# Optimization experiments

Measured on AMD Instinct MI355X. Metric: run time of the kernel, lower is better.

The kernel has to match this reference:

```python
import jax, jax.numpy as jnp
import numpy as np
import math
from jax import lax

D = 256      # d_model = out_channel
NH = 8       # n_heads
DEP = D // NH
DFF = 1024
B = 48       # conv batch == attended axis in this model
CIN = 32
HW = 32
S = 30 * 30  # (HW-2)**2 after 3x3 valid conv
OUT = 1
FMAX = float(np.finfo(np.float32).max)


def _p(k, shp, scale=0.02):
    return jax.random.normal(k, shp, jnp.float32) * scale


def setup_inputs():
    key = jax.random.key(0)
    ks = jax.random.split(key, 34)
    return {
        'X_en': jax.random.normal(ks[0], (B, CIN, HW, HW), jnp.float32),
        'X_de': jax.random.normal(ks[1], (B, CIN, HW, HW), jnp.float32),
        'conv1_w': _p(ks[2], (D, CIN, 3, 3)), 'conv1_b': _p(ks[3], (D,)),
        'conv2_w': _p(ks[4], (D, D, 3, 3)), 'conv2_b': _p(ks[5], (D,)),
        'enc_wq': _p(ks[6], (D, D)), 'enc_wk': _p(ks[7], (D, D)), 'enc_wv': _p(ks[8], (D, D)),
        'enc_rel_w': _p(ks[9], (S, NH, DEP, B)),
        'enc_ffn_w1': _p(ks[10], (DFF, D)), 'enc_ffn_b1': _p(ks[11], (DFF,)),
        'enc_ffn_w2': _p(ks[12], (D, DFF)), 'enc_ffn_b2': _p(ks[13], (D,)),
        'dec_m_wq': _p(ks[14], (D, D)), 'dec_m_wk': _p(ks[15], (D, D)), 'dec_m_wv': _p(ks[16], (D, D)),
        'dec_m_rel_w': _p(ks[17], (S, NH, DEP, B)),
        'dec_m_lin1_w': _p(ks[18], (B, B)), 'dec_m_lin1_b': _p(ks[19], (B,)),
        'dec_m_lin2_w': _p(ks[20], (B, B)), 'dec_m_lin2_b': _p(ks[21], (B,)),
        'dec_c_wq': _p(ks[22], (D, D)), 'dec_c_wk': _p(ks[23], (D, D)), 'dec_c_wv': _p(ks[24], (D, D)),
        'dec_c_rel_w': _p(ks[25], (S, NH, DEP, B)),
        'dec_ffn_w1': _p(ks[26], (DFF, D)), 'dec_ffn_b1': _p(ks[27], (DFF,)),
        'dec_ffn_w2': _p(ks[28], (D, DFF)), 'dec_ffn_b2': _p(ks[29], (D,)),
        'out_w': _p(ks[30], (OUT, D)), 'out_b': _p(ks[31], (OUT,)),
    }


def _ln(x, eps=1e-5):
    m = jnp.mean(x, -1, keepdims=True)
    v = jnp.mean((x - m) ** 2, -1, keepdims=True)
    return (x - m) / jnp.sqrt(v + eps)


def _skew(q, w):
    # Music-Transformer relative-position skew: matmul + pad + reshape + slice
    emd = jnp.einsum('shbd,shdj->shbj', q, w)  # (S,NH,b,b)
    s, h, i, j = emd.shape
    l = i + j - 1
    x = jnp.concatenate([emd, jnp.zeros_like(emd)], -1).reshape(s, h, -1)
    pad = (-x.shape[-1]) % l
    x = jnp.pad(x, ((0, 0), (0, 0), (0, pad)))
    return x.reshape(s, h, -1, l)[:, :, :i, i - 1:]


def _mha(xq, xk, xv, wq, wk, wv, rel_w, lins=None):
    b, sl, d = xq.shape
    # raw view (not transpose): (b,sl,d) -> (sl,b,NH,DEP), then swap to (sl,NH,b,DEP)
    q = (xq @ wq.T).reshape(sl, b, NH, DEP).swapaxes(1, 2)
    k = (xk @ wk.T).reshape(sl, b, NH, DEP).swapaxes(1, 2)
    v = (xv @ wv.T).reshape(sl, b, NH, DEP).swapaxes(1, 2)
    scores = jnp.einsum('shid,shjd->shij', q, k) / math.sqrt(DEP)  # (sl,NH,b,b)
    if lins is not None:  # masked path: per-call linears + causal mask
        l1w, l1b, l2w, l2b = lins
        qk = scores @ l1w.T + l1b
        qk = jnp.swapaxes(qk, 2, 3) @ l2w.T + l2b
        mask = jnp.triu(jnp.full((b, b), -FMAX, jnp.float32), 1)
        bmm = qk + mask
    else:
        bmm = scores  # linear1/linear2 outputs are discarded when mask=False
    attn = jax.nn.softmax(bmm + _skew(q, rel_w), axis=0)  # softmax over dim 0 (S)
    out = jnp.einsum('shij,shjd->shid', attn, v)  # (sl,NH,b,DEP)
    return out.reshape(b, sl, NH * DEP)  # view(a_s[2], a_s[0], -1)


def reference(X_en, X_de, conv1_w, conv1_b, conv2_w, conv2_b, enc_wq, enc_wk, enc_wv, enc_rel_w, enc_ffn_w1, enc_ffn_b1, enc_ffn_w2, enc_ffn_b2, dec_m_wq, dec_m_wk, dec_m_wv, dec_m_rel_w, dec_m_lin1_w, dec_m_lin1_b, dec_m_lin2_w, dec_m_lin2_b, dec_c_wq, dec_c_wk, dec_c_wv, dec_c_rel_w, dec_ffn_w1, dec_ffn_b1, dec_ffn_w2, dec_ffn_b2, out_w, out_b):
    def conv(x, w, b_, pad):
        y = lax.conv_general_dilated(x, w, (1, 1), [(pad, pad), (pad, pad)],
                                     dimension_numbers=('NCHW', 'OIHW', 'NCHW'))
        return y + b_[None, :, None, None]

    def convs(x):
        return conv(conv(x, conv1_w, conv1_b, 0), conv2_w, conv2_b, 1)

    xpe = convs(X_en)
    xpd = convs(X_de)
    b, d, h, w = xpe.shape
    x_en = xpe.reshape(b, h * w, d)  # raw reshape as in torch source
    x_de = xpd.reshape(b, h * w, d)
    # encoder layer
    a = _mha(x_en, x_en, x_en, enc_wq, enc_wk, enc_wv, enc_rel_w)
    o1 = _ln(x_en + a)
    f = jax.nn.relu(o1 @ enc_ffn_w1.T + enc_ffn_b1) @ enc_ffn_w2.T + enc_ffn_b2
    enc_out = _ln(o1 + f)
    # decoder layer
    m = _mha(x_de, x_de, x_de, dec_m_wq, dec_m_wk, dec_m_wv, dec_m_rel_w,
             (dec_m_lin1_w, dec_m_lin1_b, dec_m_lin2_w, dec_m_lin2_b))
    h1 = _ln(x_de + m)
    c = _mha(h1, enc_out, enc_out, dec_c_wq, dec_c_wk, dec_c_wv, dec_c_rel_w)
    h2 = _ln(c + h1)
    f2 = jax.nn.relu(h2 @ dec_ffn_w1.T + dec_ffn_b1) @ dec_ffn_w2.T + dec_ffn_b2
    h3 = _ln(h2 + f2)
    y = h3 @ out_w.T + out_b
    return jax.nn.softmax(y, axis=0)
```

## Files before the change

### kernel.cpp

```cpp
#include <hip/hip_runtime.h>
#include <float.h>

typedef __bf16 bf16;
typedef __attribute__((ext_vector_type(8))) __bf16 bf16x8;
typedef __attribute__((ext_vector_type(4))) __bf16 bf16x4;
typedef __attribute__((ext_vector_type(4))) float f32x4;

__device__ __forceinline__ int imin(int a, int b) { return a < b ? a : b; }

__device__ __forceinline__ void gl2lds(const bf16* g, bf16* l) {
  __builtin_amdgcn_global_load_lds(
      (const __attribute__((address_space(1))) void*)g,
      (__attribute__((address_space(3))) void*)l, 16, 0, 0);
}

__global__ void k_zero(bf16* zp) { zp[threadIdx.x] = (bf16)0.0f; }

struct CastSegs { const float* s[13]; bf16* d[13]; int n[13]; };
__global__ void k_cast_all(CastSegs sg, int total) {
  int i = blockIdx.x * 256 + threadIdx.x;
  if (i >= total) return;
  for (int k = 0; k < 13; ++k) {
    if (i < sg.n[k]) { sg.d[k][i] = (bf16)sg.s[k][i]; return; }
    i -= sg.n[k];
  }
}

__global__ void k_prep_x(const float* __restrict__ X, bf16* __restrict__ XR) {
  int idx = blockIdx.x * 256 + threadIdx.x;
  if (idx >= 48 * 1024 * 32) return;
  int b = idx >> 15, r = idx & 32767, pos = r >> 5, ic = r & 31;
  XR[idx] = (bf16)X[((size_t)(b * 32 + ic) << 10) + pos];
}

__global__ void k_pack_conv(const float* __restrict__ w, bf16* __restrict__ dst,
                            int OC, int IC, int total) {
  int idx = blockIdx.x * 256 + threadIdx.x;
  if (idx >= total) return;
  int t = idx / (OC * IC);
  int rem = idx - t * OC * IC;
  int oc = rem / IC, ic = rem - oc * IC;
  dst[idx] = (bf16)w[(size_t)(oc * IC + ic) * 9 + t];
}

__global__ __launch_bounds__(256, 2) void k_gemm128(
    const bf16* __restrict__ A, const bf16* __restrict__ B,
    const float* __restrict__ bias, bf16* __restrict__ C,
    int M, int N, int K, int relu, int ldc, int coff) {
  __shared__ alignas(16) bf16 SM[8192];
  bf16* As = SM;
  bf16* Bs = SM + 4096;
  const int t = threadIdx.x, wave = t >> 6;
  const int lane = t & 63, fr = lane & 15, kq = lane >> 4;
  const int wm = wave & 1, wn = wave >> 1;
  const int m0 = blockIdx.x * 128, n0 = blockIdx.y * 128;
  const int srow = t >> 2, kseg = (t & 3) * 8;
  f32x4 acc[4][4] = {};
  const bf16* gA0 = A + (size_t)imin(m0 + srow, M - 1) * K + kseg;
  const bf16* gA1 = A + (size_t)imin(m0 + 64 + srow, M - 1) * K + kseg;
  const bf16* gB0 = B + (size_t)(n0 + srow) * K + kseg;
  const bf16* gB1 = B + (size_t)(n0 + 64 + srow) * K + kseg;
  bf16* sA0 = As + wave * 512;
  bf16* sA1 = As + 2048 + wave * 512;
  bf16* sB0 = Bs + wave * 512;
  bf16* sB1 = Bs + 2048 + wave * 512;
  for (int k0 = 0; k0 < K; k0 += 32) {
    gl2lds(gA0 + k0, sA0);
    gl2lds(gA1 + k0, sA1);
    gl2lds(gB0 + k0, sB0);
    gl2lds(gB1 + k0, sB1);
    __syncthreads();
    bf16x8 af[4], bw[4];
    for (int mt = 0; mt < 4; ++mt)
      af[mt] = *(const bf16x8*)(As + (wm * 64 + mt * 16 + fr) * 32 + kq * 8);
    for (int nt = 0; nt < 4; ++nt)
      bw[nt] = *(const bf16x8*)(Bs + (wn * 64 + nt * 16 + fr) * 32 + kq * 8);
    for (int mt = 0; mt < 4; ++mt)
      for (int nt = 0; nt < 4; ++nt)
        acc[mt][nt] = __builtin_amdgcn_mfma_f32_16x16x32_bf16(af[mt], bw[nt], acc[mt][nt], 0, 0, 0);
    __syncthreads();
  }
  bf16* Cst = SM;
  for (int half = 0; half < 2; ++half) {
    if (wm == half) {
      for (int mt = 0; mt < 4; ++mt)
        for (int nt = 0; nt < 4; ++nt) {
          int n = n0 + wn * 64 + nt * 16 + fr;
          float bv = bias ? bias[n] : 0.0f;
          for (int r = 0; r < 4; ++r) {
            float v = acc[mt][nt][r] + bv;
            if (relu) v = fmaxf(v, 0.0f);
            Cst[(mt * 16 + kq * 4 + r) * 128 + wn * 64 + nt * 16 + fr] = (bf16)v;
          }
        }
    }
    __syncthreads();
    for (int i = t; i < 1024; i += 256) {
      int r = i >> 4, cs = i & 15;
      int gm = m0 + half * 64 + r;
      if (gm < M)
        *(bf16x8*)(C + (size_t)gm * ldc + coff + n0 + cs * 8) = *(const bf16x8*)(Cst + r * 128 + cs * 8);
    }
    __syncthreads();
  }
}

template <int CIN, int PAD, int SRCW, int SRCROWS, int CHECK, int TRANS>
__global__ __launch_bounds__(256, 2) void k_conv128(
    const bf16* __restrict__ A, const bf16* __restrict__ Bp,
    const float* __restrict__ bias, bf16* __restrict__ C,
    const bf16* __restrict__ zpage) {
  __shared__ alignas(16) bf16 SM[8192];
  bf16* As = SM;
  bf16* Bs = SM + 4096;
  const int t = threadIdx.x, wave = t >> 6;
  const int lane = t & 63, fr = lane & 15, kq = lane >> 4;
  const int wm = wave & 1, wn = wave >> 1;
  const int m0 = blockIdx.x * 128, n0 = blockIdx.y * 128;
  const int srow = t >> 2, kseg = (t & 3) * 8;
  f32x4 acc[4][4] = {};
  int bb[2], yy[2], xx[2];
  for (int hf = 0; hf < 2; ++hf) {
    int m = imin(m0 + hf * 64 + srow, 43199);
    int b = m / 900, p = m - b * 900;
    bb[hf] = b; yy[hf] = p / 30; xx[hf] = p - (p / 30) * 30;
  }
  bf16* sA0 = As + wave * 512;
  bf16* sA1 = As + 2048 + wave * 512;
  bf16* sB0 = Bs + wave * 512;
  bf16* sB1 = Bs + 2048 + wave * 512;
  for (int t9 = 0; t9 < 9; ++t9) {
    const int ky = t9 / 3, kx = t9 - ky * 3;
    const bf16* ga[2];
    for (int hf = 0; hf < 2; ++hf) {
      int sy = yy[hf] + ky - PAD, sx = xx[hf] + kx - PAD;
      bool valid = !CHECK || (sy >= 0 && sy < SRCW && sx >= 0 && sx < SRCW);
      ga[hf] = (valid ? A + (size_t)(bb[hf] * SRCROWS + sy * SRCW + sx) * CIN : zpage) + kseg;
    }
    const bf16* gb = Bp + (size_t)(t9 * 256 + n0 + srow) * CIN + kseg;
    for (int k0 = 0; k0 < CIN; k0 += 32) {
      gl2lds(ga[0] + k0, sA0);
      gl2lds(ga[1] + k0, sA1);
      gl2lds(gb + k0, sB0);
      gl2lds(gb + (size_t)64 * CIN + k0, sB1);
      __syncthreads();
      bf16x8 af[4], bw[4];
      for (int mt = 0; mt < 4; ++mt)
        af[mt] = *(const bf16x8*)(As + (wm * 64 + mt * 16 + fr) * 32 + kq * 8);
      for (int nt = 0; nt < 4; ++nt)
        bw[nt] = *(const bf16x8*)(Bs + (wn * 64 + nt * 16 + fr) * 32 + kq * 8);
      for (int mt = 0; mt < 4; ++mt)
        for (int nt = 0; nt < 4; ++nt)
          acc[mt][nt] = __builtin_amdgcn_mfma_f32_16x16x32_bf16(af[mt], bw[nt], acc[mt][nt], 0, 0, 0);
      __syncthreads();
    }
  }
  bf16* Cst = SM;
  for (int half = 0; half < 2; ++half) {
    if (wm == half) {
      for (int mt = 0; mt < 4; ++mt)
        for (int nt = 0; nt < 4; ++nt) {
          int n = n0 + wn * 64 + nt * 16 + fr;
          float bv = bias[n];
          for (int r = 0; r < 4; ++r) {
            float v = acc[mt][nt][r] + bv;
            if (TRANS)
              Cst[(wn * 64 + nt * 16 + fr) * 64 + mt * 16 + kq * 4 + r] = (bf16)v;
            else
              Cst[(mt * 16 + kq * 4 + r) * 128 + wn * 64 + nt * 16 + fr] = (bf16)v;
          }
        }
    }
    __syncthreads();
    if (TRANS) {
      for (int i = t; i < 2048; i += 256) {
        int oc = i >> 4, pc = i & 15;
        int gm = m0 + half * 64 + pc * 4;
        if (gm < 43200) {
          int b = gm / 900, p = gm - b * 900;
          *(bf16x4*)(C + (size_t)(b * 256 + n0 + oc) * 900 + p) = *(const bf16x4*)(Cst + oc * 64 + pc * 4);
        }
      }
    } else {
      for (int i = t; i < 1024; i += 256) {
        int r = i >> 4, cs = i & 15;
        int gm = m0 + half * 64 + r;
        if (gm < 43200)
          *(bf16x8*)(C + (size_t)gm * 256 + n0 + cs * 8) = *(const bf16x8*)(Cst + r * 128 + cs * 8);
      }
    }
    __syncthreads();
  }
}

template <int MASKED>
__global__ __launch_bounds__(256, MASKED ? 3 : 4) void k_attn_z(
    const bf16* __restrict__ QKV, const float* __restrict__ relw, bf16* __restrict__ Z,
    const float* __restrict__ l1w, const float* __restrict__ l1b,
    const float* __restrict__ l2w, const float* __restrict__ l2b) {
  __shared__ alignas(16) bf16 Rt[48 * 40];
  __shared__ float EMD[48 * 49];
  __shared__ alignas(16) bf16 zst[48 * 48];
  __shared__ alignas(16) bf16 Sc[MASKED ? 48 * 72 : 8];
  __shared__ alignas(16) bf16 L1b[MASKED ? 48 * 72 : 8];
  __shared__ alignas(16) bf16 L2b[MASKED ? 48 * 72 : 8];
  __shared__ alignas(16) bf16 T2b[MASKED ? 48 * 72 : 8];
  const int sh = blockIdx.x, s = sh >> 3, h = sh & 7;
  const int t = threadIdx.x, wave = t >> 6, lane = t & 63, fr = lane & 15, kq = lane >> 4;
  const float scale = 0.17677669529663687f;
  if constexpr (MASKED) {
    for (int i = t; i < 48 * 72; i += 256) {
      int r = i / 72, c = i - r * 72;
      bf16 z0 = (bf16)0.0f;
      L1b[i] = (c < 48) ? (bf16)l1w[r * 48 + c] : z0;
      L2b[i] = (c < 48) ? (bf16)l2w[r * 48 + c] : z0;
      Sc[i] = z0;
      T2b[i] = z0;
    }
  }
  {
    const float* rb = relw + (size_t)sh * 1536;
    for (int i = t; i < 1536; i += 256) {
      int k = i / 48, j = i - k * 48;
      Rt[j * 40 + k] = (bf16)rb[i];
    }
  }
  __syncthreads();
  f32x4 sreg[3];
  int u = 0;
  for (int t9 = wave; t9 < 9; t9 += 4, ++u) {
    int ti = t9 / 3, tj = t9 - ti * 3;
    bf16x8 af = *(const bf16x8*)(QKV + (size_t)(s * 48 + ti * 16 + fr) * 768 + h * 32 + kq * 8);
    bf16x8 bk = *(const bf16x8*)(QKV + (size_t)(s * 48 + tj * 16 + fr) * 768 + 256 + h * 32 + kq * 8);
    bf16x8 rf = *(const bf16x8*)(Rt + (tj * 16 + fr) * 40 + kq * 8);
    f32x4 sacc = {}, eacc = {};
    sacc = __builtin_amdgcn_mfma_f32_16x16x32_bf16(af, bk, sacc, 0, 0, 0);
    eacc = __builtin_amdgcn_mfma_f32_16x16x32_bf16(af, rf, eacc, 0, 0, 0);
    for (int r = 0; r < 4; ++r)
      EMD[(ti * 16 + kq * 4 + r) * 49 + tj * 16 + fr] = eacc[r];
    if constexpr (MASKED) {
      for (int r = 0; r < 4; ++r)
        Sc[(ti * 16 + kq * 4 + r) * 72 + tj * 16 + fr] = (bf16)(sacc[r] * scale);
    } else {
      for (int r = 0; r < 4; ++r) sreg[u][r] = sacc[r] * scale;
    }
  }
  __syncthreads();
  if constexpr (!MASKED) {
    u = 0;
    for (int t9 = wave; t9 < 9; t9 += 4, ++u) {
      int ti = t9 / 3, tj = t9 - ti * 3;
      for (int r = 0; r < 4; ++r) {
        int i = ti * 16 + kq * 4 + r, j = tj * 16 + fr;
        float v = sreg[u][r];
        if (j <= i) v += EMD[i * 49 + 47 + j - i];
        zst[i * 48 + j] = (bf16)v;
      }
    }
  } else {
    for (int t9 = wave; t9 < 9; t9 += 4) {
      int ti = t9 / 3, tj = t9 - ti * 3;
      f32x4 a2 = {};
      for (int k0 = 0; k0 < 64; k0 += 32) {
        bf16x8 af = *(const bf16x8*)(Sc + (ti * 16 + fr) * 72 + k0 + kq * 8);
        bf16x8 bw = *(const bf16x8*)(L1b + (tj * 16 + fr) * 72 + k0 + kq * 8);
        a2 = __builtin_amdgcn_mfma_f32_16x16x32_bf16(af, bw, a2, 0, 0, 0);
      }
      for (int r = 0; r < 4; ++r) {
        int i = ti * 16 + kq * 4 + r, a = tj * 16 + fr;
        T2b[a * 72 + i] = (bf16)(a2[r] + l1b[a]);
      }
    }
    __syncthreads();
    for (int t9 = wave; t9 < 9; t9 += 4) {
      int ti = t9 / 3, tj = t9 - ti * 3;
      f32x4 a2 = {};
      for (int k0 = 0; k0 < 64; k0 += 32) {
        bf16x8 af = *(const bf16x8*)(T2b + (ti * 16 + fr) * 72 + k0 + kq * 8);
        bf16x8 bw = *(const bf16x8*)(L2b + (tj * 16 + fr) * 72 + k0 + kq * 8);
        a2 = __builtin_amdgcn_mfma_f32_16x16x32_bf16(af, bw, a2, 0, 0, 0);
      }
      for (int r = 0; r < 4; ++r) {
        int aa = ti * 16 + kq * 4 + r, cc = tj * 16 + fr;
        float v;
        if (cc > aa) v = -10000.0f;
        else v = a2[r] + l2b[cc] + EMD[aa * 49 + 47 + cc - aa];
        zst[aa * 48 + cc] = (bf16)v;
      }
    }
  }
  __syncthreads();
  bf16* zb = Z + (size_t)sh * 2304;
  for (int c = t; c < 288; c += 256)
    *(bf16x8*)(zb + c * 8) = *(const bf16x8*)(zst + c * 8);
}

__global__ __launch_bounds__(256) void k_colstats(const bf16* __restrict__ Z,
                                                  float* __restrict__ Mc, float* __restrict__ Ic) {
  __shared__ float rm[4][64], rs[4][64];
  const int t = threadIdx.x, tc = t & 63, sg = t >> 6;
  const int col = blockIdx.x * 64 + tc;
  const bf16* p = Z + col;
  float m = -FLT_MAX, ssum = 0.0f;
  for (int s = sg * 225; s < sg * 225 + 225; ++s) {
    float v = (float)p[(size_t)s * 18432];
    if (v > m) { ssum *= __expf(m - v); m = v; }
    ssum += __expf(v - m);
  }
  rm[sg][tc] = m; rs[sg][tc] = ssum;
  __syncthreads();
  if (sg == 0) {
    float M2 = fmaxf(fmaxf(rm[0][tc], rm[1][tc]), fmaxf(rm[2][tc], rm[3][tc]));
    float S2 = 0.0f;
    for (int g = 0; g < 4; ++g) S2 += rs[g][tc] * __expf(rm[g][tc] - M2);
    Mc[col] = M2;
    Ic[col] = 1.0f / S2;
  }
}

__global__ __launch_bounds__(256, 4) void k_attn_av(
    const bf16* __restrict__ Z, const bf16* __restrict__ QKV,
    const float* __restrict__ Mc, const float* __restrict__ Ic, bf16* __restrict__ O) {
  __shared__ alignas(16) bf16 Ps[48 * 72];
  __shared__ alignas(16) bf16 Vt[32 * 72];
  __shared__ alignas(16) bf16 Ost[48 * 32];
  const int sh = blockIdx.x, s = sh >> 3, h = sh & 7;
  const int t = threadIdx.x, wave = t >> 6, lane = t & 63, fr = lane & 15, kq = lane >> 4;
  for (int i = t; i < 48 * 72; i += 256) Ps[i] = (bf16)0.0f;
  for (int i = t; i < 32 * 72; i += 256) Vt[i] = (bf16)0.0f;
  __syncthreads();
  const bf16* zb = Z + (size_t)sh * 2304;
  const float* mc = Mc + h * 2304;
  const float* ic = Ic + h * 2304;
  for (int c = t; c < 288; c += 256) {
    int r = c / 6, seg = c - r * 6;
    int idx = r * 48 + seg * 8;
    bf16x8 zv = *(const bf16x8*)(zb + idx);
    f32x4 m0v = *(const f32x4*)(mc + idx), m1v = *(const f32x4*)(mc + idx + 4);
    f32x4 i0v = *(const f32x4*)(ic + idx), i1v = *(const f32x4*)(ic + idx + 4);
    bf16x8 pv;
    for (int e = 0; e < 4; ++e) pv[e] = (bf16)(__expf((float)zv[e] - m0v[e]) * i0v[e]);
    for (int e = 0; e < 4; ++e) pv[4 + e] = (bf16)(__expf((float)zv[4 + e] - m1v[e]) * i1v[e]);
    *(bf16x8*)(Ps + r * 72 + seg * 8) = pv;
  }
  for (int i = t; i < 1536; i += 256) {
    int j = i >> 5, d = i & 31;
    Vt[d * 72 + j] = QKV[(size_t)(s * 48 + j) * 768 + 512 + h * 32 + d];
  }
  __syncthreads();
  for (int t6 = wave; t6 < 6; t6 += 4) {
    int ti = t6 >> 1, td = t6 & 1;
    f32x4 a2 = {};
    for (int k0 = 0; k0 < 64; k0 += 32) {
      bf16x8 af = *(const bf16x8*)(Ps + (ti * 16 + fr) * 72 + k0 + kq * 8);
      bf16x8 bv = *(const bf16x8*)(Vt + (td * 16 + fr) * 72 + k0 + kq * 8);
      a2 = __builtin_amdgcn_mfma_f32_16x16x32_bf16(af, bv, a2, 0, 0, 0);
    }
    for (int r = 0; r < 4; ++r)
      Ost[(ti * 16 + kq * 4 + r) * 32 + td * 16 + fr] = (bf16)a2[r];
  }
  __syncthreads();
  bf16* ob = O + (size_t)sh * 1536;
  for (int c = t; c < 192; c += 256)
    *(bf16x8*)(ob + c * 8) = *(const bf16x8*)(Ost + c * 8);
}

__global__ __launch_bounds__(256) void k_add_ln(
    const bf16* __restrict__ Xa, const bf16* __restrict__ Xb, bf16* __restrict__ out) {
  const int t = threadIdx.x, lane = t & 63, w = t >> 6;
  const size_t off = ((size_t)blockIdx.x * 4 + w) * 256 + lane * 4;
  bf16x4 av = *(const bf16x4*)(Xa + off);
  bf16x4 bv = *(const bf16x4*)(Xb + off);
  f32x4 x;
  for (int c = 0; c < 4; ++c) x[c] = (float)av[c] + (float)bv[c];
  float sum = x[0] + x[1] + x[2] + x[3];
  for (int o = 1; o < 64; o <<= 1) sum += __shfl_xor(sum, o);
  float mean = sum * (1.0f / 256.0f);
  float q = 0.0f;
  for (int c = 0; c < 4; ++c) { float d = x[c] - mean; q += d * d; }
  for (int o = 1; o < 64; o <<= 1) q += __shfl_xor(q, o);
  float rstd = rsqrtf(q * (1.0f / 256.0f) + 1e-5f);
  bf16x4 y;
  for (int c = 0; c < 4; ++c) y[c] = (bf16)((x[c] - mean) * rstd);
  *(bf16x4*)(out + off) = y;
}

__global__ __launch_bounds__(256) void k_ydot(
    const bf16* __restrict__ H, const float* __restrict__ w,
    const float* __restrict__ b, float* __restrict__ Y) {
  const int t = threadIdx.x, lane = t & 63, wv = t >> 6;
  const size_t row = (size_t)blockIdx.x * 4 + wv;
  bf16x4 hx = *(const bf16x4*)(H + row * 256 + lane * 4);
  f32x4 ww = *(const f32x4*)(w + lane * 4);
  float s = (float)hx[0] * ww[0] + (float)hx[1] * ww[1] + (float)hx[2] * ww[2] + (float)hx[3] * ww[3];
  for (int o = 1; o < 64; o <<= 1) s += __shfl_xor(s, o);
  if (lane == 0) Y[row] = s + b[0];
}

__global__ void k_softmax48(const float* __restrict__ Y, float* __restrict__ O) {
  int ss = blockIdx.x * 256 + threadIdx.x;
  if (ss >= 900) return;
  float m = -FLT_MAX;
  for (int b = 0; b < 48; ++b) m = fmaxf(m, Y[b * 900 + ss]);
  float sum = 0.0f;
  for (int b = 0; b < 48; ++b) sum += __expf(Y[b * 900 + ss] - m);
  float inv = 1.0f / sum;
  for (int b = 0; b < 48; ++b) O[b * 900 + ss] = __expf(Y[b * 900 + ss] - m) * inv;
}

extern "C" void kernel_launch(void* const* d_in, const int* in_sizes, int n_in,
                              void* d_out, int out_size, void* d_ws, size_t ws_size,
                              hipStream_t stream) {
  (void)in_sizes; (void)n_in; (void)out_size;
  const float* X_en = (const float*)d_in[0];
  const float* X_de = (const float*)d_in[1];
  const float* conv1_w = (const float*)d_in[2];
  const float* conv1_b = (const float*)d_in[3];
  const float* conv2_w = (const float*)d_in[4];
  const float* conv2_b = (const float*)d_in[5];
  const float* enc_wq = (const float*)d_in[6];
  const float* enc_wk = (const float*)d_in[7];
  const float* enc_wv = (const float*)d_in[8];
  const float* enc_rel = (const float*)d_in[9];
  const float* enc_f1w = (const float*)d_in[10];
  const float* enc_f1b = (const float*)d_in[11];
  const float* enc_f2w = (const float*)d_in[12];
  const float* enc_f2b = (const float*)d_in[13];
  const float* dm_wq = (const float*)d_in[14];
  const float* dm_wk = (const float*)d_in[15];
  const float* dm_wv = (const float*)d_in[16];
  const float* dm_rel = (const float*)d_in[17];
  const float* dm_l1w = (const float*)d_in[18];
  const float* dm_l1b = (const float*)d_in[19];
  const float* dm_l2w = (const float*)d_in[20];
  const float* dm_l2b = (const float*)d_in[21];
  const float* dc_wq = (const float*)d_in[22];
  const float* dc_wk = (const float*)d_in[23];
  const float* dc_wv = (const float*)d_in[24];
  const float* dc_rel = (const float*)d_in[25];
  const float* d_f1w = (const float*)d_in[26];
  const float* d_f1b = (const float*)d_in[27];
  const float* d_f2w = (const float*)d_in[28];
  const float* d_f2b = (const float*)d_in[29];
  const float* out_w = (const float*)d_in[30];
  const float* out_b = (const float*)d_in[31];
  float* OUT = (float*)d_out;

  const size_t SLOT = 22118400;
  char* ws = (char*)d_ws;
  size_t o = 0;
  bf16* S1 = (bf16*)(ws + o); o += SLOT;
  bf16* S2 = (bf16*)(ws + o); o += SLOT;
  bf16* S3 = (bf16*)(ws + o); o += SLOT;
  bf16* S4 = (bf16*)(ws + o); o += SLOT;
  bf16* S5 = (bf16*)(ws + o); o += SLOT;
  char* U = ws + o; o += 33177600 + 3 * SLOT;
  bf16* Zb = (bf16*)U;
  bf16* QKV = (bf16*)(U + 33177600);
  bf16* XR = (bf16*)U;
  bf16* C1R = (bf16*)(U + 3145728);
  bf16* HID = (bf16*)U;
  bf16* wa = (bf16*)(ws + o); o += 4603904;
  float* Y = (float*)(ws + o); o += 172800;
  if (ws_size < o) return;

  bf16* zpage = (bf16*)Y;
  float* encM = (float*)S4; float* encI = encM + 18432;
  float* dmM  = (float*)S3; float* dmI  = dmM + 18432;
  float* crM  = (float*)S2; float* crI  = crM + 18432;

  bf16* c1p = wa;
  bf16* c2p = wa + 73728;
  bf16* EQKVw = wa + 663552;
  bf16* MQKVw = wa + 860160;
  bf16* cqw = wa + 1056768;
  bf16* CKVw = wa + 1122304;
  bf16* ef1 = wa + 1253376;
  bf16* ef2 = wa + 1515520;
  bf16* df1 = wa + 1777664;
  bf16* df2 = wa + 2039808;

  auto gemm = [&](const bf16* A, const bf16* B, const float* bias, bf16* C,
                  int M, int N, int K, int relu, int ldc, int coff) {
    k_gemm128<<<dim3((M + 127) / 128, N / 128), dim3(256), 0, stream>>>(
        A, B, bias, C, M, N, K, relu, ldc, coff);
  };

  k_zero<<<dim3(1), dim3(256), 0, stream>>>(zpage);
  k_pack_conv<<<dim3(288), dim3(256), 0, stream>>>(conv1_w, c1p, 256, 32, 73728);
  k_pack_conv<<<dim3(2304), dim3(256), 0, stream>>>(conv2_w, c2p, 256, 256, 589824);
  {
    CastSegs sg;
    const float* srcs[13] = {enc_wq, enc_wk, enc_wv, dm_wq, dm_wk, dm_wv, dc_wq,
                             dc_wk, dc_wv, enc_f1w, enc_f2w, d_f1w, d_f2w};
    bf16* dsts[13] = {EQKVw, EQKVw + 65536, EQKVw + 131072, MQKVw, MQKVw + 65536,
                      MQKVw + 131072, cqw, CKVw, CKVw + 65536, ef1, ef2, df1, df2};
    int ns[13] = {65536, 65536, 65536, 65536, 65536, 65536, 65536, 65536, 65536,
                  262144, 262144, 262144, 262144};
    int total = 0;
    for (int k = 0; k < 13; ++k) { sg.s[k] = srcs[k]; sg.d[k] = dsts[k]; sg.n[k] = ns[k]; total += ns[k]; }
    k_cast_all<<<dim3((total + 255) / 256), dim3(256), 0, stream>>>(sg, total);
  }

  auto conv_chain = [&](const float* X, bf16* outB) {
    k_prep_x<<<dim3(6144), dim3(256), 0, stream>>>(X, XR);
    k_conv128<32, 0, 32, 1024, 0, 0><<<dim3(338, 2), dim3(256), 0, stream>>>(XR, c1p, conv1_b, C1R, zpage);
    k_conv128<256, 1, 30, 900, 1, 1><<<dim3(338, 2), dim3(256), 0, stream>>>(C1R, c2p, conv2_b, outB, zpage);
  };
  conv_chain(X_en, S1);
  conv_chain(X_de, S2);

  gemm(S1, EQKVw, nullptr, QKV, 43200, 768, 256, 0, 768, 0);
  k_attn_z<0><<<dim3(7200), dim3(256), 0, stream>>>(QKV, enc_rel, Zb, nullptr, nullptr, nullptr, nullptr);
  k_colstats<<<dim3(288), dim3(256), 0, stream>>>(Zb, encM, encI);
  k_attn_av<<<dim3(7200), dim3(256), 0, stream>>>(Zb, QKV, encM, encI, S5);
  k_add_ln<<<dim3(10800), dim3(256), 0, stream>>>(S1, S5, S3);
  gemm(S3, ef1, enc_f1b, HID, 43200, 1024, 256, 1, 1024, 0);
  gemm(HID, ef2, enc_f2b, S5, 43200, 256, 1024, 0, 256, 0);
  k_add_ln<<<dim3(10800), dim3(256), 0, stream>>>(S3, S5, S1);

  gemm(S2, MQKVw, nullptr, QKV, 43200, 768, 256, 0, 768, 0);
  k_attn_z<1><<<dim3(7200), dim3(256), 0, stream>>>(QKV, dm_rel, Zb, dm_l1w, dm_l1b, dm_l2w, dm_l2b);
  k_colstats<<<dim3(288), dim3(256), 0, stream>>>(Zb, dmM, dmI);
  k_attn_av<<<dim3(7200), dim3(256), 0, stream>>>(Zb, QKV, dmM, dmI, S5);
  k_add_ln<<<dim3(10800), dim3(256), 0, stream>>>(S2, S5, S4);

  gemm(S4, cqw, nullptr, QKV, 43200, 256, 256, 0, 768, 0);
  gemm(S1, CKVw, nullptr, QKV, 43200, 512, 256, 0, 768, 256);
  k_attn_z<0><<<dim3(7200), dim3(256), 0, stream>>>(QKV, dc_rel, Zb, nullptr, nullptr, nullptr, nullptr);
  k_colstats<<<dim3(288), dim3(256), 0, stream>>>(Zb, crM, crI);
  k_attn_av<<<dim3(7200), dim3(256), 0, stream>>>(Zb, QKV, crM, crI, S5);
  k_add_ln<<<dim3(10800), dim3(256), 0, stream>>>(S5, S4, S3);

  gemm(S3, df1, d_f1b, HID, 43200, 1024, 256, 1, 1024, 0);
  gemm(HID, df2, d_f2b, S5, 43200, 256, 1024, 0, 256, 0);
  k_add_ln<<<dim3(10800), dim3(256), 0, stream>>>(S3, S5, S4);
  k_ydot<<<dim3(10800), dim3(256), 0, stream>>>(S4, out_w, out_b, Y);
  k_softmax48<<<dim3(4), dim3(256), 0, stream>>>(Y, OUT);
}
```

Measured before the change: 1.131 ms.

## Pre-transpose relative weights, stage Q/K in LDS, and widen colstats parallelism

Adds a separate kernel that converts and transposes each attention's relative-position weights to bf16 once, and another that packs the decoder mask linear weights once. The attention-score kernel then reads these directly instead of converting per block, and stages Q/K tiles in LDS with vector loads. It also drops full LDS zero-fills in favour of padding-only clears, raises occupancy bounds, vectorises the V transpose load, and splits column statistics across 4x more blocks. The cost is an extra pass over the relative weights plus scratch buffers that alias existing workspace.

```diff
diff --git a/kernel.cpp b/kernel.cpp
--- a/kernel.cpp
+++ b/kernel.cpp
@@ -23,6 +23,24 @@
   for (int k = 0; k < 13; ++k) {
     if (i < sg.n[k]) { sg.d[k][i] = (bf16)sg.s[k][i]; return; }
     i -= sg.n[k];
+  }
+}
+
+__global__ void k_prep_rel(const float* __restrict__ rel, bf16* __restrict__ RelT) {
+  int idx = blockIdx.x * 256 + threadIdx.x;
+  if (idx >= 7200 * 1536) return;
+  int sh = idx >> 9;  sh /= 3;
+  int r = idx - sh * 1536;
+  int j = r >> 5, k = r & 31;
+  RelT[idx] = (bf16)rel[(size_t)sh * 1536 + k * 48 + j];
+}
+
+__global__ void k_prep_lin(const float* __restrict__ l1w, const float* __restrict__ l2w,
+                           bf16* __restrict__ L1p, bf16* __restrict__ L2p) {
+  for (int i = threadIdx.x; i < 3456; i += 256) {
+    int r = i / 72, c = i - r * 72;
+    L1p[i] = (c < 48) ? (bf16)l1w[r * 48 + c] : (bf16)0.0f;
+    L2p[i] = (c < 48) ? (bf16)l2w[r * 48 + c] : (bf16)0.0f;
   }
 }
 
@@ -194,45 +212,40 @@
 }
 
 template <int MASKED>
-__global__ __launch_bounds__(256, MASKED ? 3 : 4) void k_attn_z(
-    const bf16* __restrict__ QKV, const float* __restrict__ relw, bf16* __restrict__ Z,
-    const float* __restrict__ l1w, const float* __restrict__ l1b,
-    const float* __restrict__ l2w, const float* __restrict__ l2b) {
-  __shared__ alignas(16) bf16 Rt[48 * 40];
+__global__ __launch_bounds__(256, MASKED ? 4 : 5) void k_attn_z(
+    const bf16* __restrict__ QKV, const bf16* __restrict__ RelT, bf16* __restrict__ Z,
+    const bf16* __restrict__ L1p, const bf16* __restrict__ L2p,
+    const float* __restrict__ l1b, const float* __restrict__ l2b) {
+  __shared__ alignas(16) bf16 QKs[2][48 * 40];
   __shared__ float EMD[48 * 49];
   __shared__ alignas(16) bf16 zst[48 * 48];
   __shared__ alignas(16) bf16 Sc[MASKED ? 48 * 72 : 8];
-  __shared__ alignas(16) bf16 L1b[MASKED ? 48 * 72 : 8];
-  __shared__ alignas(16) bf16 L2b[MASKED ? 48 * 72 : 8];
   __shared__ alignas(16) bf16 T2b[MASKED ? 48 * 72 : 8];
   const int sh = blockIdx.x, s = sh >> 3, h = sh & 7;
   const int t = threadIdx.x, wave = t >> 6, lane = t & 63, fr = lane & 15, kq = lane >> 4;
   const float scale = 0.17677669529663687f;
+  for (int c = t; c < 384; c += 256) {
+    int half = c >= 192 ? 1 : 0, cc = c - half * 192;
+    int row = cc >> 2, seg = cc & 3;
+    *(bf16x8*)(&QKs[half][row * 40 + seg * 8]) =
+        *(const bf16x8*)(QKV + (size_t)(s * 48 + row) * 768 + half * 256 + h * 32 + seg * 8);
+  }
   if constexpr (MASKED) {
-    for (int i = t; i < 48 * 72; i += 256) {
-      int r = i / 72, c = i - r * 72;
-      bf16 z0 = (bf16)0.0f;
-      L1b[i] = (c < 48) ? (bf16)l1w[r * 48 + c] : z0;
-      L2b[i] = (c < 48) ? (bf16)l2w[r * 48 + c] : z0;
-      Sc[i] = z0;
-      T2b[i] = z0;
-    }
-  }
-  {
-    const float* rb = relw + (size_t)sh * 1536;
-    for (int i = t; i < 1536; i += 256) {
-      int k = i / 48, j = i - k * 48;
-      Rt[j * 40 + k] = (bf16)rb[i];
+    for (int i = t; i < 768; i += 256) {
+      int r = i >> 4, c = 48 + (i & 15);
+      Sc[r * 72 + c] = (bf16)0.0f;
+      T2b[r * 72 + c] = (bf16)0.0f;
     }
   }
   __syncthreads();
+  const bf16* relb = RelT + (size_t)sh * 1536;
   f32x4 sreg[3];
   int u = 0;
   for (int t9 = wave; t9 < 9; t9 += 4, ++u) {
     int ti = t9 / 3, tj = t9 - ti * 3;
-    bf16x8 af = *(const bf16x8*)(QKV + (size_t)(s * 48 + ti * 16 + fr) * 768 + h * 32 + kq * 8);
-    bf16x8 bk = *(const bf16x8*)(QKV + (size_t)(s * 48 + tj * 16 + fr) * 768 + 256 + h * 32 + kq * 8);
-    bf16x8 rf = *(const bf16x8*)(Rt + (tj * 16 + fr) * 40 + kq * 8);
+    bf16x8 af = *(const bf16x8*)(&QKs[0][(ti * 16 + fr) * 40 + kq * 8]);
+    bf16x8 bk = *(const bf16x8*)(&QKs[1][(tj * 16 + fr) * 40 + kq * 8]);
+    bf16x8 rf = *(const bf16x8*)(relb + (tj * 16 + fr) * 32 + kq * 8);
     f32x4 sacc = {}, eacc = {};
     sacc = __builtin_amdgcn_mfma_f32_16x16x32_bf16(af, bk, sacc, 0, 0, 0);
     eacc = __builtin_amdgcn_mfma_f32_16x16x32_bf16(af, rf, eacc, 0, 0, 0);
@@ -263,7 +276,7 @@
       f32x4 a2 = {};
       for (int k0 = 0; k0 < 64; k0 += 32) {
         bf16x8 af = *(const bf16x8*)(Sc + (ti * 16 + fr) * 72 + k0 + kq * 8);
-        bf16x8 bw = *(const bf16x8*)(L1b + (tj * 16 + fr) * 72 + k0 + kq * 8);
+        bf16x8 bw = *(const bf16x8*)(L1p + (tj * 16 + fr) * 72 + k0 + kq * 8);
         a2 = __builtin_amdgcn_mfma_f32_16x16x32_bf16(af, bw, a2, 0, 0, 0);
       }
       for (int r = 0; r < 4; ++r) {
@@ -277,7 +290,7 @@
       f32x4 a2 = {};
       for (int k0 = 0; k0 < 64; k0 += 32) {
         bf16x8 af = *(const bf16x8*)(T2b + (ti * 16 + fr) * 72 + k0 + kq * 8);
-        bf16x8 bw = *(const bf16x8*)(L2b + (tj * 16 + fr) * 72 + k0 + kq * 8);
+        bf16x8 bw = *(const bf16x8*)(L2p + (tj * 16 + fr) * 72 + k0 + kq * 8);
         a2 = __builtin_amdgcn_mfma_f32_16x16x32_bf16(af, bw, a2, 0, 0, 0);
       }
       for (int r = 0; r < 4; ++r) {
@@ -297,28 +310,30 @@
 
 __global__ __launch_bounds__(256) void k_colstats(const bf16* __restrict__ Z,
                                                   float* __restrict__ Mc, float* __restrict__ Ic) {
-  __shared__ float rm[4][64], rs[4][64];
-  const int t = threadIdx.x, tc = t & 63, sg = t >> 6;
-  const int col = blockIdx.x * 64 + tc;
+  __shared__ float rm[16][17], rs[16][17];
+  const int t = threadIdx.x, tc = t & 15, sg = t >> 4;
+  const int col = blockIdx.x * 16 + tc;
   const bf16* p = Z + col;
+  const int s0 = sg * 57, s1 = imin(900, s0 + 57);
   float m = -FLT_MAX, ssum = 0.0f;
-  for (int s = sg * 225; s < sg * 225 + 225; ++s) {
+  for (int s = s0; s < s1; ++s) {
     float v = (float)p[(size_t)s * 18432];
     if (v > m) { ssum *= __expf(m - v); m = v; }
     ssum += __expf(v - m);
   }
   rm[sg][tc] = m; rs[sg][tc] = ssum;
   __syncthreads();
-  if (sg == 0) {
-    float M2 = fmaxf(fmaxf(rm[0][tc], rm[1][tc]), fmaxf(rm[2][tc], rm[3][tc]));
+  if (t < 16) {
+    float M2 = -FLT_MAX;
+    for (int g = 0; g < 16; ++g) M2 = fmaxf(M2, rm[g][t]);
     float S2 = 0.0f;
-    for (int g = 0; g < 4; ++g) S2 += rs[g][tc] * __expf(rm[g][tc] - M2);
-    Mc[col] = M2;
-    Ic[col] = 1.0f / S2;
-  }
-}
-
-__global__ __launch_bounds__(256, 4) void k_attn_av(
+    for (int g = 0; g < 16; ++g) S2 += rs[g][t] * __expf(rm[g][t] - M2);
+    Mc[blockIdx.x * 16 + t] = M2;
+    Ic[blockIdx.x * 16 + t] = 1.0f / S2;
+  }
+}
+
+__global__ __launch_bounds__(256, 6) void k_attn_av(
     const bf16* __restrict__ Z, const bf16* __restrict__ QKV,
     const float* __restrict__ Mc, const float* __restrict__ Ic, bf16* __restrict__ O) {
   __shared__ alignas(16) bf16 Ps[48 * 72];
@@ -326,9 +341,8 @@
   __shared__ alignas(16) bf16 Ost[48 * 32];
   const int sh = blockIdx.x, s = sh >> 3, h = sh & 7;
   const int t = threadIdx.x, wave = t >> 6, lane = t & 63, fr = lane & 15, kq = lane >> 4;
-  for (int i = t; i < 48 * 72; i += 256) Ps[i] = (bf16)0.0f;
-  for (int i = t; i < 32 * 72; i += 256) Vt[i] = (bf16)0.0f;
-  __syncthreads();
+  for (int i = t; i < 768; i += 256) Ps[(i >> 4) * 72 + 48 + (i & 15)] = (bf16)0.0f;
+  for (int i = t; i < 512; i += 256) Vt[(i >> 4) * 72 + 48 + (i & 15)] = (bf16)0.0f;
   const bf16* zb = Z + (size_t)sh * 2304;
   const float* mc = Mc + h * 2304;
   const float* ic = Ic + h * 2304;
@@ -343,9 +357,10 @@
     for (int e = 0; e < 4; ++e) pv[4 + e] = (bf16)(__expf((float)zv[4 + e] - m1v[e]) * i1v[e]);
     *(bf16x8*)(Ps + r * 72 + seg * 8) = pv;
   }
-  for (int i = t; i < 1536; i += 256) {
-    int j = i >> 5, d = i & 31;
-    Vt[d * 72 + j] = QKV[(size_t)(s * 48 + j) * 768 + 512 + h * 32 + d];
+  for (int c = t; c < 192; c += 256) {
+    int j = c >> 2, seg = c & 3;
+    bf16x8 v = *(const bf16x8*)(QKV + (size_t)(s * 48 + j) * 768 + 512 + h * 32 + seg * 8);
+    for (int e = 0; e < 8; ++e) Vt[(seg * 8 + e) * 72 + j] = v[e];
   }
   __syncthreads();
   for (int t6 = wave; t6 < 6; t6 += 4) {
@@ -460,7 +475,7 @@
   bf16* XR = (bf16*)U;
   bf16* C1R = (bf16*)(U + 3145728);
   bf16* HID = (bf16*)U;
-  bf16* wa = (bf16*)(ws + o); o += 4603904;
+  bf16* wa = (bf16*)(ws + o); o += 4603904 + 16384;
   float* Y = (float*)(ws + o); o += 172800;
   if (ws_size < o) return;
 
@@ -468,6 +483,9 @@
   float* encM = (float*)S4; float* encI = encM + 18432;
   float* dmM  = (float*)S3; float* dmI  = dmM + 18432;
   float* crM  = (float*)S2; float* crI  = crM + 18432;
+  bf16* encRel = S3;
+  bf16* dmRel  = S5;
+  bf16* crRel  = S3;
 
   bf16* c1p = wa;
   bf16* c2p = wa + 73728;
@@ -479,6 +497,8 @@
   bf16* ef2 = wa + 1515520;
   bf16* df1 = wa + 1777664;
   bf16* df2 = wa + 2039808;
+  bf16* L1p = wa + 2301952;
+  bf16* L2p = wa + 2305408;
 
   auto gemm = [&](const bf16* A, const bf16* B, const float* bias, bf16* C,
                   int M, int N, int K, int relu, int ldc, int coff) {
@@ -489,6 +509,7 @@
   k_zero<<<dim3(1), dim3(256), 0, stream>>>(zpage);
   k_pack_conv<<<dim3(288), dim3(256), 0, stream>>>(conv1_w, c1p, 256, 32, 73728);
   k_pack_conv<<<dim3(2304), dim3(256), 0, stream>>>(conv2_w, c2p, 256, 256, 589824);
+  k_prep_lin<<<dim3(1), dim3(256), 0, stream>>>(dm_l1w, dm_l2w, L1p, L2p);
   {
     CastSegs sg;
     const float* srcs[13] = {enc_wq, enc_wk, enc_wv, dm_wq, dm_wk, dm_wv, dc_wq,
@@ -511,8 +532,9 @@
   conv_chain(X_de, S2);
 
   gemm(S1, EQKVw, nullptr, QKV, 43200, 768, 256, 0, 768, 0);
-  k_attn_z<0><<<dim3(7200), dim3(256), 0, stream>>>(QKV, enc_rel, Zb, nullptr, nullptr, nullptr, nullptr);
-  k_colstats<<<dim3(288), dim3(256), 0, stream>>>(Zb, encM, encI);
+  k_prep_rel<<<dim3(43200), dim3(256), 0, stream>>>(enc_rel, encRel);
+  k_attn_z<0><<<dim3(7200), dim3(256), 0, stream>>>(QKV, encRel, Zb, nullptr, nullptr, nullptr, nullptr);
+  k_colstats<<<dim3(1152), dim3(256), 0, stream>>>(Zb, encM, encI);
   k_attn_av<<<dim3(7200), dim3(256), 0, stream>>>(Zb, QKV, encM, encI, S5);
   k_add_ln<<<dim3(10800), dim3(256), 0, stream>>>(S1, S5, S3);
   gemm(S3, ef1, enc_f1b, HID, 43200, 1024, 256, 1, 1024, 0);
@@ -520,15 +542,17 @@
   k_add_ln<<<dim3(10800), dim3(256), 0, stream>>>(S3, S5, S1);
 
   gemm(S2, MQKVw, nullptr, QKV, 43200, 768, 256, 0, 768, 0);
-  k_attn_z<1><<<dim3(7200), dim3(256), 0, stream>>>(QKV, dm_rel, Zb, dm_l1w, dm_l1b, dm_l2w, dm_l2b);
-  k_colstats<<<dim3(288), dim3(256), 0, stream>>>(Zb, dmM, dmI);
+  k_prep_rel<<<dim3(43200), dim3(256), 0, stream>>>(dm_rel, dmRel);
+  k_attn_z<1><<<dim3(7200), dim3(256), 0, stream>>>(QKV, dmRel, Zb, L1p, L2p, dm_l1b, dm_l2b);
+  k_colstats<<<dim3(1152), dim3(256), 0, stream>>>(Zb, dmM, dmI);
   k_attn_av<<<dim3(7200), dim3(256), 0, stream>>>(Zb, QKV, dmM, dmI, S5);
   k_add_ln<<<dim3(10800), dim3(256), 0, stream>>>(S2, S5, S4);
 
   gemm(S4, cqw, nullptr, QKV, 43200, 256, 256, 0, 768, 0);
   gemm(S1, CKVw, nullptr, QKV, 43200, 512, 256, 0, 768, 256);
-  k_attn_z<0><<<dim3(7200), dim3(256), 0, stream>>>(QKV, dc_rel, Zb, nullptr, nullptr, nullptr, nullptr);
-  k_colstats<<<dim3(288), dim3(256), 0, stream>>>(Zb, crM, crI);
+  k_prep_rel<<<dim3(43200), dim3(256), 0, stream>>>(dc_rel, crRel);
+  k_attn_z<0><<<dim3(7200), dim3(256), 0, stream>>>(QKV, crRel, Zb, nullptr, nullptr, nullptr, nullptr);
+  k_colstats<<<dim3(1152), dim3(256), 0, stream>>>(Zb, crM, crI);
   k_attn_av<<<dim3(7200), dim3(256), 0, stream>>>(Zb, QKV, crM, crI, S5);
   k_add_ln<<<dim3(10800), dim3(256), 0, stream>>>(S5, S4, S3);
 
```

New measurement: 1.125 ms. No clear change (-0.5%).
